# Performance work log

Measured on AMD Instinct MI355X. Metric: run time of the kernel, lower is better.

The kernel has to match this reference:

```python
import jax, jax.numpy as jnp
import numpy as np
import math

B = 4096
INPUT_SIZE = 2048
HIDDEN_SIZE = 2048


def setup_inputs() -> dict:
    key = jax.random.key(0)
    ks = jax.random.split(key, 7)
    std = 1.0 / math.sqrt(HIDDEN_SIZE)
    u = lambda k, shape: jax.random.uniform(k, shape, jnp.float32, -std, std)
    return {
        "input": jax.random.normal(ks[0], (B, INPUT_SIZE), jnp.float32),
        "hx": jax.random.normal(ks[1], (B, HIDDEN_SIZE), jnp.float32),
        "cx": jax.random.normal(ks[2], (B, HIDDEN_SIZE), jnp.float32),
        "W_x2h": u(ks[3], (4 * HIDDEN_SIZE, INPUT_SIZE)),
        "b_x2h": u(ks[4], (4 * HIDDEN_SIZE,)),
        "W_h2h": u(ks[5], (4 * HIDDEN_SIZE, HIDDEN_SIZE)),
        "b_h2h": u(ks[6], (4 * HIDDEN_SIZE,)),
    }


def reference(input, hx, cx, W_x2h, b_x2h, W_h2h, b_h2h):
    # gates: [B, 4H] = x @ W_x2h^T + b + h @ W_h2h^T + b
    gates = input @ W_x2h.T + b_x2h + hx @ W_h2h.T + b_h2h
    H = HIDDEN_SIZE
    ft = jax.nn.sigmoid(gates[:, 0 * H:1 * H])
    it = jax.nn.sigmoid(gates[:, 1 * H:2 * H])
    ct = jnp.tanh(gates[:, 2 * H:3 * H])
    ot = jax.nn.sigmoid(gates[:, 3 * H:4 * H])
    cy = ft * cx + it * ct
    hy = ot * jnp.tanh(cy)
    return (hy, cy)
```

## Files before the change

kernel.cpp:

```cpp
#include <hip/hip_runtime.h>
#include <hip/hip_bf16.h>


#define BATCH 4096
#define HID   2048
#define KDIM  2048
#define K4    4096
#define BM    128
#define BK    64
#define LDK   72

typedef __attribute__((ext_vector_type(8))) short  short8;
typedef __attribute__((ext_vector_type(4))) float  f32x4;

__device__ __forceinline__ float sigm(float x)  { return 1.f / (1.f + __expf(-x)); }
__device__ __forceinline__ float tanhx(float x) { return 2.f / (1.f + __expf(-2.f * x)) - 1.f; }

__device__ __forceinline__ uint2 pk_bf16x4(float4 v) {
  __hip_bfloat162 lo = __float22bfloat162_rn(make_float2(v.x, v.y));
  __hip_bfloat162 hi = __float22bfloat162_rn(make_float2(v.z, v.w));
  uint2 r;
  r.x = *(unsigned*)&lo;
  r.y = *(unsigned*)&hi;
  return r;
}

__device__ __forceinline__ void gload16(const void* g, void* l) {
  __builtin_amdgcn_global_load_lds(
      (const __attribute__((address_space(1))) unsigned int*)g,
      (__attribute__((address_space(3))) unsigned int*)l, 16, 0, 0);
}

__global__ __launch_bounds__(256) void conv_a(const float* __restrict__ X,
                                              const float* __restrict__ Hx,
                                              short* __restrict__ A) {
  const int gid = blockIdx.x * 256 + threadIdx.x;
  const int m   = gid >> 9;
  const int pos = (gid & 511) << 3;
  const float* src = (pos < KDIM) ? X  + (size_t)m * KDIM + pos
                                  : Hx + (size_t)m * KDIM + (pos - KDIM);
  float4 v0 = *(const float4*)src;
  float4 v1 = *(const float4*)(src + 4);
  uint2 p0 = pk_bf16x4(v0), p1 = pk_bf16x4(v1);
  uint4 o; o.x = p0.x; o.y = p0.y; o.z = p1.x; o.w = p1.y;
  *(uint4*)(A + (size_t)gid * 8) = o;
}

__global__ __launch_bounds__(256) void conv_b(const float* __restrict__ Wx,
                                              const float* __restrict__ Wh,
                                              short* __restrict__ Bm) {
  const int gid = blockIdx.x * 256 + threadIdx.x;
  const int jp  = gid >> 9;
  const int pos = (gid & 511) << 3;
  const int srow = (jp & 3) * HID + (jp >> 2);
  const float* src = (pos < KDIM) ? Wx + (size_t)srow * KDIM + pos
                                  : Wh + (size_t)srow * KDIM + (pos - KDIM);
  float4 v0 = *(const float4*)src;
  float4 v1 = *(const float4*)(src + 4);
  uint2 p0 = pk_bf16x4(v0), p1 = pk_bf16x4(v1);
  uint4 o; o.x = p0.x; o.y = p0.y; o.z = p1.x; o.w = p1.y;
  *(uint4*)(Bm + (size_t)gid * 8) = o;
}

__global__ __launch_bounds__(256) void lstm_mm(
    const short* __restrict__ A, const short* __restrict__ Bm,
    const float* __restrict__ Cx,
    const float* __restrict__ bx, const float* __restrict__ bh,
    float* __restrict__ Hy, float* __restrict__ Cy)
{
  __shared__ __align__(16) short A_lds[BM * BK];
  __shared__ __align__(16) short B_lds[BM * BK];

  const int tid  = threadIdx.x;
  const int wv   = tid >> 6;
  const int lane = tid & 63;
  const int quad = lane >> 4;
  const int ln   = lane & 15;
  const int wm   = wv >> 1;
  const int wn   = wv & 1;
  const int m0   = blockIdx.x * BM;
  const int j0   = blockIdx.y * BM;
  const int h0   = blockIdx.y * 32;

  f32x4 acc[4][4];
  #pragma unroll
  for (int a = 0; a < 4; ++a)
    #pragma unroll
    for (int b = 0; b < 4; ++b)
      acc[a][b] = (f32x4){0.f, 0.f, 0.f, 0.f};

  const int srow = lane >> 3;
  const int slot = lane & 7;
  const int sx   = ((slot ^ srow) << 3);
  const short* ag = A  + (size_t)(m0 + wv * 32 + srow) * K4 + sx;
  const short* bg = Bm + (size_t)(j0 + wv * 32 + srow) * K4 + sx;
  short* al = &A_lds[wv * 32 * BK];
  short* bl = &B_lds[wv * 32 * BK];

  for (int t = 0; t < K4 / BK; ++t) {
    const int k0 = t * BK;
    __syncthreads();
    #pragma unroll
    for (int i = 0; i < 4; ++i) {
      gload16(ag + k0 + i * 8 * K4, al + i * 8 * BK);
      gload16(bg + k0 + i * 8 * K4, bl + i * 8 * BK);
    }
    __syncthreads();
    #pragma unroll
    for (int ks = 0; ks < 2; ++ks) {
      short8 af[4], bfv[4];
      #pragma unroll
      for (int u = 0; u < 4; ++u) {
        const int ar = wm * 64 + u * 16 + ln;
        af[u]  = *(const short8*)&A_lds[ar * BK + (((ks * 4 + quad) ^ (ar & 7)) << 3)];
      }
      #pragma unroll
      for (int u = 0; u < 4; ++u) {
        const int br = wn * 64 + u * 16 + ln;
        bfv[u] = *(const short8*)&B_lds[br * BK + (((ks * 4 + quad) ^ (br & 7)) << 3)];
      }
      #pragma unroll
      for (int tm = 0; tm < 4; ++tm)
        #pragma unroll
        for (int tn = 0; tn < 4; ++tn)
          acc[tm][tn] = __builtin_amdgcn_mfma_f32_16x16x32_bf16(
              af[tm], bfv[tn], acc[tm][tn], 0, 0, 0);
    }
  }

  const int g = lane & 3;
  float biasv[4];
  int   hgs[4];
  #pragma unroll
  for (int tn = 0; tn < 4; ++tn) {
    int c  = wn * 64 + tn * 16 + ln;
    int hg = h0 + (c >> 2);
    hgs[tn] = hg;
    int j = g * HID + hg;
    biasv[tn] = bx[j] + bh[j];
  }
  #pragma unroll
  for (int tm = 0; tm < 4; ++tm) {
    #pragma unroll
    for (int r = 0; r < 4; ++r) {
      int mrow = m0 + wm * 64 + tm * 16 + quad * 4 + r;
      #pragma unroll
      for (int tn = 0; tn < 4; ++tn) {
        float v   = acc[tm][tn][r] + biasv[tn];
        float act = (g == 2) ? tanhx(v) : sigm(v);
        float y1 = __shfl_xor(act, 1);
        float y2 = __shfl_xor(act, 2);
        float y3 = __shfl_xor(act, 3);
        float ft = (g == 0) ? act : ((g == 1) ? y1 : ((g == 2) ? y2 : y3));
        float it = (g == 1) ? act : ((g == 0) ? y1 : ((g == 3) ? y2 : y3));
        float gt = (g == 2) ? act : ((g == 3) ? y1 : ((g == 0) ? y2 : y3));
        float ot = (g == 3) ? act : ((g == 2) ? y1 : ((g == 1) ? y2 : y3));
        if (g < 2) {
          size_t off = (size_t)mrow * HID + hgs[tn];
          float cxv = Cx[off];
          float cyv = ft * cxv + it * gt;
          if (g == 0) Hy[off] = ot * tanhx(cyv);
          else        Cy[off] = cyv;
        }
      }
    }
  }
}

__global__ __launch_bounds__(256) void lstm_cell_fallback(
    const float* __restrict__ X, const float* __restrict__ Hx,
    const float* __restrict__ Cx,
    const float* __restrict__ Wx, const float* __restrict__ bx,
    const float* __restrict__ Wh, const float* __restrict__ bh,
    float* __restrict__ Hy, float* __restrict__ Cy)
{
  __shared__ __align__(16) short A_lds[BM * LDK];
  __shared__ __align__(16) short B_lds[BM * LDK];

  const int tid  = threadIdx.x;
  const int wv   = tid >> 6;
  const int lane = tid & 63;
  const int quad = lane >> 4;
  const int ln   = lane & 15;
  const int wm   = wv >> 1;
  const int wn   = wv & 1;
  const int m0   = blockIdx.x * BM;
  const int h0   = blockIdx.y * 32;

  f32x4 acc[4][4];
  #pragma unroll
  for (int a = 0; a < 4; ++a)
    #pragma unroll
    for (int b = 0; b < 4; ++b)
      acc[a][b] = (f32x4){0.f, 0.f, 0.f, 0.f};

  const int rA  = tid >> 4;
  const int kc4 = (tid & 15) * 4;
  size_t aoff[8], boff[8];
  int    lrow[8];
  #pragma unroll
  for (int q = 0; q < 8; ++q) {
    int row  = q * 16 + rA;
    lrow[q]  = row;
    aoff[q]  = (size_t)(m0 + row) * KDIM + kc4;
    int wrow = (row & 3) * HID + h0 + (row >> 2);
    boff[q]  = (size_t)wrow * KDIM + kc4;
  }

  const int NT = 2 * (KDIM / BK);
  float4 areg[8], breg[8];
  #pragma unroll
  for (int q = 0; q < 8; ++q) {
    areg[q] = *(const float4*)(X  + aoff[q]);
    breg[q] = *(const float4*)(Wx + boff[q]);
  }

  for (int t = 0; t < NT; ++t) {
    __syncthreads();
    #pragma unroll
    for (int q = 0; q < 8; ++q) {
      *(uint2*)&A_lds[lrow[q] * LDK + kc4] = pk_bf16x4(areg[q]);
      *(uint2*)&B_lds[lrow[q] * LDK + kc4] = pk_bf16x4(breg[q]);
    }
    __syncthreads();
    if (t + 1 < NT) {
      const float* Ap = (t + 1 < 32) ? X  : Hx;
      const float* Wp = (t + 1 < 32) ? Wx : Wh;
      const int k0 = ((t + 1) & 31) * BK;
      #pragma unroll
      for (int q = 0; q < 8; ++q) {
        areg[q] = *(const float4*)(Ap + aoff[q] + k0);
        breg[q] = *(const float4*)(Wp + boff[q] + k0);
      }
    }
    #pragma unroll
    for (int ks = 0; ks < 2; ++ks) {
      short8 af[4], bfv[4];
      #pragma unroll
      for (int u = 0; u < 4; ++u)
        af[u] = *(const short8*)&A_lds[(wm * 64 + u * 16 + ln) * LDK + ks * 32 + quad * 8];
      #pragma unroll
      for (int u = 0; u < 4; ++u)
        bfv[u] = *(const short8*)&B_lds[(wn * 64 + u * 16 + ln) * LDK + ks * 32 + quad * 8];
      #pragma unroll
      for (int tm = 0; tm < 4; ++tm)
        #pragma unroll
        for (int tn = 0; tn < 4; ++tn)
          acc[tm][tn] = __builtin_amdgcn_mfma_f32_16x16x32_bf16(
              af[tm], bfv[tn], acc[tm][tn], 0, 0, 0);
    }
  }

  const int g = lane & 3;
  float biasv[4];
  int   hgs[4];
  #pragma unroll
  for (int tn = 0; tn < 4; ++tn) {
    int c  = wn * 64 + tn * 16 + ln;
    int hg = h0 + (c >> 2);
    hgs[tn] = hg;
    int j = g * HID + hg;
    biasv[tn] = bx[j] + bh[j];
  }
  #pragma unroll
  for (int tm = 0; tm < 4; ++tm) {
    #pragma unroll
    for (int r = 0; r < 4; ++r) {
      int mrow = m0 + wm * 64 + tm * 16 + quad * 4 + r;
      #pragma unroll
      for (int tn = 0; tn < 4; ++tn) {
        float v   = acc[tm][tn][r] + biasv[tn];
        float act = (g == 2) ? tanhx(v) : sigm(v);
        float y1 = __shfl_xor(act, 1);
        float y2 = __shfl_xor(act, 2);
        float y3 = __shfl_xor(act, 3);
        float ft = (g == 0) ? act : ((g == 1) ? y1 : ((g == 2) ? y2 : y3));
        float it = (g == 1) ? act : ((g == 0) ? y1 : ((g == 3) ? y2 : y3));
        float gt = (g == 2) ? act : ((g == 3) ? y1 : ((g == 0) ? y2 : y3));
        float ot = (g == 3) ? act : ((g == 2) ? y1 : ((g == 1) ? y2 : y3));
        if (g < 2) {
          size_t off = (size_t)mrow * HID + hgs[tn];
          float cxv = Cx[off];
          float cyv = ft * cxv + it * gt;
          if (g == 0) Hy[off] = ot * tanhx(cyv);
          else        Cy[off] = cyv;
        }
      }
    }
  }
}

extern "C" void kernel_launch(void* const* d_in, const int* in_sizes, int n_in,
                              void* d_out, int out_size, void* d_ws, size_t ws_size,
                              hipStream_t stream) {
  const float* X  = (const float*)d_in[0];
  const float* Hx = (const float*)d_in[1];
  const float* Cx = (const float*)d_in[2];
  const float* Wx = (const float*)d_in[3];
  const float* bx = (const float*)d_in[4];
  const float* Wh = (const float*)d_in[5];
  const float* bh = (const float*)d_in[6];
  float*       Hy = (float*)d_out;
  float*       Cy = Hy + (size_t)BATCH * HID;

  const size_t needA = (size_t)BATCH * K4 * sizeof(short);
  const size_t needB = (size_t)(4 * HID) * K4 * sizeof(short);

  if (d_ws != nullptr && ws_size >= needA + needB) {
    short* Abf = (short*)d_ws;
    short* Bbf = (short*)((char*)d_ws + needA);
    conv_a<<<dim3((BATCH * (K4 / 8)) / 256), dim3(256), 0, stream>>>(X, Hx, Abf);
    conv_b<<<dim3((4 * HID * (K4 / 8)) / 256), dim3(256), 0, stream>>>(Wx, Wh, Bbf);
    dim3 grid(BATCH / BM, HID / 32, 1);
    lstm_mm<<<grid, dim3(256, 1, 1), 0, stream>>>(Abf, Bbf, Cx, bx, bh, Hy, Cy);
  } else {
    dim3 grid(BATCH / BM, HID / 32, 1);
    lstm_cell_fallback<<<grid, dim3(256, 1, 1), 0, stream>>>(X, Hx, Cx, Wx, bx, Wh, bh, Hy, Cy);
  }
}
```

Measured before the change: 586.0 us.

## Replace GEMM with 256x256-tile 8-wave kernel using double-buffered LDS pipeline

Result: faster. 571.7 us (-2.4%).

```diff
diff --git a/kernel.cpp b/kernel.cpp
--- a/kernel.cpp
+++ b/kernel.cpp
@@ -6,8 +6,6 @@
 #define HID   2048
 #define KDIM  2048
 #define K4    4096
-#define BM    128
-#define BK    64
 #define LDK   72
 
 typedef __attribute__((ext_vector_type(8))) short  short8;
@@ -30,6 +28,10 @@
       (const __attribute__((address_space(1))) unsigned int*)g,
       (__attribute__((address_space(3))) unsigned int*)l, 16, 0, 0);
 }
+
+#define BAR()  asm volatile("s_barrier" ::: "memory")
+#define LGK0() asm volatile("s_waitcnt lgkmcnt(0)" ::: "memory")
+#define VMC(n) asm volatile("s_waitcnt vmcnt(" #n ")" ::: "memory")
 
 __global__ __launch_bounds__(256) void conv_a(const float* __restrict__ X,
                                               const float* __restrict__ Hx,
@@ -62,14 +64,190 @@
   *(uint4*)(Bm + (size_t)gid * 8) = o;
 }
 
-__global__ __launch_bounds__(256) void lstm_mm(
+__device__ __forceinline__ void lda4(short8 (&dst)[8], const short* base,
+                                     int arow, int sx0, int sx1, int mfb) {
+  #pragma unroll
+  for (int u = 0; u < 4; ++u) {
+    dst[u]     = *(const short8*)&base[arow + (mfb + u) * 1024 + sx0];
+    dst[4 + u] = *(const short8*)&base[arow + (mfb + u) * 1024 + sx1];
+  }
+}
+__device__ __forceinline__ void ldb2(short8 (&dst)[4], const short* base,
+                                     int brow, int sx0, int sx1, int nfb) {
+  #pragma unroll
+  for (int v = 0; v < 2; ++v) {
+    dst[v]     = *(const short8*)&base[brow + (nfb + v) * 1024 + sx0];
+    dst[2 + v] = *(const short8*)&base[brow + (nfb + v) * 1024 + sx1];
+  }
+}
+__device__ __forceinline__ void mmq(f32x4 (&acc)[8][4], const short8 (&A)[8],
+                                    const short8 (&B)[4], int MB, int NB) {
+  __builtin_amdgcn_s_setprio(1);
+  #pragma unroll
+  for (int ks = 0; ks < 2; ++ks)
+    #pragma unroll
+    for (int u = 0; u < 4; ++u)
+      #pragma unroll
+      for (int v = 0; v < 2; ++v)
+        acc[MB + u][NB + v] = __builtin_amdgcn_mfma_f32_16x16x32_bf16(
+            A[ks * 4 + u], B[ks * 2 + v], acc[MB + u][NB + v], 0, 0, 0);
+  __builtin_amdgcn_s_setprio(0);
+}
+
+__global__ __launch_bounds__(512, 2) void lstm_mm8(
     const short* __restrict__ A, const short* __restrict__ Bm,
     const float* __restrict__ Cx,
     const float* __restrict__ bx, const float* __restrict__ bh,
     float* __restrict__ Hy, float* __restrict__ Cy)
 {
-  __shared__ __align__(16) short A_lds[BM * BK];
-  __shared__ __align__(16) short B_lds[BM * BK];
+  __shared__ __align__(16) short A_sh[2 * 16384];
+  __shared__ __align__(16) short B_sh[2 * 16384];
+
+  const int tid  = threadIdx.x;
+  const int wv   = tid >> 6;
+  const int lane = tid & 63;
+  const int quad = lane >> 4;
+  const int ln   = lane & 15;
+  const int wm   = wv >> 2;
+  const int wn   = wv & 3;
+  const int m0   = blockIdx.x * 256;
+  const int j0   = blockIdx.y * 256;
+  const int h0   = blockIdx.y * 64;
+
+  f32x4 acc[8][4];
+  #pragma unroll
+  for (int a = 0; a < 8; ++a)
+    #pragma unroll
+    for (int b = 0; b < 4; ++b)
+      acc[a][b] = (f32x4){0.f, 0.f, 0.f, 0.f};
+
+  const int l8  = lane >> 3;
+  const int swz = ((lane & 7) ^ (l8 & 7)) << 3;
+  const short* aG = A  + (size_t)(m0 + l8) * K4 + swz;
+  const short* bG = Bm + (size_t)(j0 + l8) * K4 + swz;
+
+  #define STAGE_A(d, h, tau) do {                                             \
+    gload16(aG + ((size_t)((h)*128 + wv*16    )) * K4 + (tau)*64,             \
+            &A_sh[(d)*16384 + (h)*8192 + wv*1024]);                           \
+    gload16(aG + ((size_t)((h)*128 + wv*16 + 8)) * K4 + (tau)*64,             \
+            &A_sh[(d)*16384 + (h)*8192 + wv*1024 + 512]);                     \
+  } while (0)
+  #define STAGE_B(d, h, tau) do {                                             \
+    gload16(bG + ((size_t)((h)*128 + wv*16    )) * K4 + (tau)*64,             \
+            &B_sh[(d)*16384 + (h)*8192 + wv*1024]);                           \
+    gload16(bG + ((size_t)((h)*128 + wv*16 + 8)) * K4 + (tau)*64,             \
+            &B_sh[(d)*16384 + (h)*8192 + wv*1024 + 512]);                     \
+  } while (0)
+
+  const int arow = (wm * 128 + ln) * 64;
+  const int brow = (wn * 64  + ln) * 64;
+  const int sx0  = ((0 + quad) ^ (ln & 7)) << 3;
+  const int sx1  = ((4 + quad) ^ (ln & 7)) << 3;
+
+  STAGE_A(0, 0, 0); STAGE_A(0, 1, 0); STAGE_B(0, 0, 0); STAGE_B(0, 1, 0);
+  STAGE_A(1, 0, 1); STAGE_A(1, 1, 1); STAGE_B(1, 0, 1);
+  VMC(6);
+  BAR();
+
+  short8 aQ0[8], aQ1[8], bLo[4], bHi[4];
+
+  #pragma unroll 1
+  for (int i = 0; i < 32; ++i) {
+    const int  S0 = 2 * i + 2, S1 = 2 * i + 3, T1k = 2 * i + 1;
+    const bool nl = (i != 31);
+    lda4(aQ0, &A_sh[0], arow, sx0, sx1, 0);
+    ldb2(bLo, &B_sh[0], brow, sx0, sx1, 0);
+    STAGE_B(1, 1, T1k);
+    BAR(); LGK0();
+    mmq(acc, aQ0, bLo, 0, 0);
+    BAR();
+    lda4(aQ1, &A_sh[0], arow, sx0, sx1, 4);
+    BAR(); LGK0();
+    mmq(acc, aQ1, bLo, 4, 0);
+    BAR();
+    ldb2(bHi, &B_sh[0], brow, sx0, sx1, 2);
+    if (nl) STAGE_A(0, 0, S0);
+    BAR(); LGK0();
+    mmq(acc, aQ1, bHi, 4, 2);
+    BAR();
+    if (nl) STAGE_B(0, 0, S0);
+    BAR();
+    mmq(acc, aQ0, bHi, 0, 2);
+    if (nl) { VMC(4); } else { VMC(0); }
+    BAR();
+    lda4(aQ0, &A_sh[16384], arow, sx0, sx1, 0);
+    ldb2(bLo, &B_sh[16384], brow, sx0, sx1, 0);
+    if (nl) STAGE_A(0, 1, S0);
+    BAR(); LGK0();
+    mmq(acc, aQ0, bLo, 0, 0);
+    BAR();
+    lda4(aQ1, &A_sh[16384], arow, sx0, sx1, 4);
+    if (nl) STAGE_B(0, 1, S0);
+    BAR(); LGK0();
+    mmq(acc, aQ1, bLo, 4, 0);
+    BAR();
+    ldb2(bHi, &B_sh[16384], brow, sx0, sx1, 2);
+    if (nl) STAGE_A(1, 0, S1);
+    BAR(); LGK0();
+    mmq(acc, aQ1, bHi, 4, 2);
+    BAR();
+    if (nl) { STAGE_B(1, 0, S1); STAGE_A(1, 1, S1); }
+    BAR();
+    mmq(acc, aQ0, bHi, 0, 2);
+    if (nl) { VMC(6); }
+    BAR();
+  }
+  #undef STAGE_A
+  #undef STAGE_B
+
+  const int g = lane & 3;
+  float biasv[4];
+  int   hgs[4];
+  #pragma unroll
+  for (int nf = 0; nf < 4; ++nf) {
+    int c  = wn * 64 + nf * 16 + ln;
+    int hg = h0 + (c >> 2);
+    hgs[nf] = hg;
+    int j = g * HID + hg;
+    biasv[nf] = bx[j] + bh[j];
+  }
+  #pragma unroll
+  for (int mf = 0; mf < 8; ++mf) {
+    #pragma unroll
+    for (int r = 0; r < 4; ++r) {
+      int mrow = m0 + wm * 128 + mf * 16 + quad * 4 + r;
+      #pragma unroll
+      for (int nf = 0; nf < 4; ++nf) {
+        float v   = acc[mf][nf][r] + biasv[nf];
+        float act = (g == 2) ? tanhx(v) : sigm(v);
+        float y1 = __shfl_xor(act, 1);
+        float y2 = __shfl_xor(act, 2);
+        float y3 = __shfl_xor(act, 3);
+        float ft = (g == 0) ? act : ((g == 1) ? y1 : ((g == 2) ? y2 : y3));
+        float it = (g == 1) ? act : ((g == 0) ? y1 : ((g == 3) ? y2 : y3));
+        float gt = (g == 2) ? act : ((g == 3) ? y1 : ((g == 0) ? y2 : y3));
+        float ot = (g == 3) ? act : ((g == 2) ? y1 : ((g == 1) ? y2 : y3));
+        if (g < 2) {
+          size_t off = (size_t)mrow * HID + hgs[nf];
+          float cxv = Cx[off];
+          float cyv = ft * cxv + it * gt;
+          if (g == 0) Hy[off] = ot * tanhx(cyv);
+          else        Cy[off] = cyv;
+        }
+      }
+    }
+  }
+}
+
+__global__ __launch_bounds__(256) void lstm_cell_fallback(
+    const float* __restrict__ X, const float* __restrict__ Hx,
+    const float* __restrict__ Cx,
+    const float* __restrict__ Wx, const float* __restrict__ bx,
+    const float* __restrict__ Wh, const float* __restrict__ bh,
+    float* __restrict__ Hy, float* __restrict__ Cy)
+{
+  __shared__ __align__(16) short A_lds[128 * LDK];
+  __shared__ __align__(16) short B_lds[128 * LDK];
 
   const int tid  = threadIdx.x;
   const int wv   = tid >> 6;
@@ -78,8 +256,7 @@
   const int ln   = lane & 15;
   const int wm   = wv >> 1;
   const int wn   = wv & 1;
-  const int m0   = blockIdx.x * BM;
-  const int j0   = blockIdx.y * BM;
+  const int m0   = blockIdx.x * 128;
   const int h0   = blockIdx.y * 32;
 
   f32x4 acc[4][4];
@@ -89,36 +266,54 @@
     for (int b = 0; b < 4; ++b)
       acc[a][b] = (f32x4){0.f, 0.f, 0.f, 0.f};
 
-  const int srow = lane >> 3;
-  const int slot = lane & 7;
-  const int sx   = ((slot ^ srow) << 3);
-  const short* ag = A  + (size_t)(m0 + wv * 32 + srow) * K4 + sx;
-  const short* bg = Bm + (size_t)(j0 + wv * 32 + srow) * K4 + sx;
-  short* al = &A_lds[wv * 32 * BK];
-  short* bl = &B_lds[wv * 32 * BK];
-
-  for (int t = 0; t < K4 / BK; ++t) {
-    const int k0 = t * BK;
+  const int rA  = tid >> 4;
+  const int kc4 = (tid & 15) * 4;
+  size_t aoff[8], boff[8];
+  int    lrow[8];
+  #pragma unroll
+  for (int q = 0; q < 8; ++q) {
+    int row  = q * 16 + rA;
+    lrow[q]  = row;
+    aoff[q]  = (size_t)(m0 + row) * KDIM + kc4;
+    int wrow = (row & 3) * HID + h0 + (row >> 2);
+    boff[q]  = (size_t)wrow * KDIM + kc4;
+  }
+
+  const int NT = 2 * (KDIM / 64);
+  float4 areg[8], breg[8];
+  #pragma unroll
+  for (int q = 0; q < 8; ++q) {
+    areg[q] = *(const float4*)(X  + aoff[q]);
+    breg[q] = *(const float4*)(Wx + boff[q]);
+  }
+
+  for (int t = 0; t < NT; ++t) {
     __syncthreads();
     #pragma unroll
-    for (int i = 0; i < 4; ++i) {
-      gload16(ag + k0 + i * 8 * K4, al + i * 8 * BK);
-      gload16(bg + k0 + i * 8 * K4, bl + i * 8 * BK);
+    for (int q = 0; q < 8; ++q) {
+      *(uint2*)&A_lds[lrow[q] * LDK + kc4] = pk_bf16x4(areg[q]);
+      *(uint2*)&B_lds[lrow[q] * LDK + kc4] = pk_bf16x4(breg[q]);
     }
     __syncthreads();
+    if (t + 1 < NT) {
+      const float* Ap = (t + 1 < 32) ? X  : Hx;
+      const float* Wp = (t + 1 < 32) ? Wx : Wh;
+      const int k0 = ((t + 1) & 31) * 64;
+      #pragma unroll
+      for (int q = 0; q < 8; ++q) {
+        areg[q] = *(const float4*)(Ap + aoff[q] + k0);
+        breg[q] = *(const float4*)(Wp + boff[q] + k0);
+      }
+    }
     #pragma unroll
     for (int ks = 0; ks < 2; ++ks) {
       short8 af[4], bfv[4];
       #pragma unroll
-      for (int u = 0; u < 4; ++u) {
-        const int ar = wm * 64 + u * 16 + ln;
-        af[u]  = *(const short8*)&A_lds[ar * BK + (((ks * 4 + quad) ^ (ar & 7)) << 3)];
-      }
-      #pragma unroll
-      for (int u = 0; u < 4; ++u) {
-        const int br = wn * 64 + u * 16 + ln;
-        bfv[u] = *(const short8*)&B_lds[br * BK + (((ks * 4 + quad) ^ (br & 7)) << 3)];
-      }
+      for (int u = 0; u < 4; ++u)
+        af[u] = *(const short8*)&A_lds[(wm * 64 + u * 16 + ln) * LDK + ks * 32 + quad * 8];
+      #pragma unroll
+      for (int u = 0; u < 4; ++u)
+        bfv[u] = *(const short8*)&B_lds[(wn * 64 + u * 16 + ln) * LDK + ks * 32 + quad * 8];
       #pragma unroll
       for (int tm = 0; tm < 4; ++tm)
         #pragma unroll
@@ -167,129 +362,6 @@
   }
 }
 
-__global__ __launch_bounds__(256) void lstm_cell_fallback(
-    const float* __restrict__ X, const float* __restrict__ Hx,
-    const float* __restrict__ Cx,
-    const float* __restrict__ Wx, const float* __restrict__ bx,
-    const float* __restrict__ Wh, const float* __restrict__ bh,
-    float* __restrict__ Hy, float* __restrict__ Cy)
-{
-  __shared__ __align__(16) short A_lds[BM * LDK];
-  __shared__ __align__(16) short B_lds[BM * LDK];
-
-  const int tid  = threadIdx.x;
-  const int wv   = tid >> 6;
-  const int lane = tid & 63;
-  const int quad = lane >> 4;
-  const int ln   = lane & 15;
-  const int wm   = wv >> 1;
-  const int wn   = wv & 1;
-  const int m0   = blockIdx.x * BM;
-  const int h0   = blockIdx.y * 32;
-
-  f32x4 acc[4][4];
-  #pragma unroll
-  for (int a = 0; a < 4; ++a)
-    #pragma unroll
-    for (int b = 0; b < 4; ++b)
-      acc[a][b] = (f32x4){0.f, 0.f, 0.f, 0.f};
-
-  const int rA  = tid >> 4;
-  const int kc4 = (tid & 15) * 4;
-  size_t aoff[8], boff[8];
-  int    lrow[8];
-  #pragma unroll
-  for (int q = 0; q < 8; ++q) {
-    int row  = q * 16 + rA;
-    lrow[q]  = row;
-    aoff[q]  = (size_t)(m0 + row) * KDIM + kc4;
-    int wrow = (row & 3) * HID + h0 + (row >> 2);
-    boff[q]  = (size_t)wrow * KDIM + kc4;
-  }
-
-  const int NT = 2 * (KDIM / BK);
-  float4 areg[8], breg[8];
-  #pragma unroll
-  for (int q = 0; q < 8; ++q) {
-    areg[q] = *(const float4*)(X  + aoff[q]);
-    breg[q] = *(const float4*)(Wx + boff[q]);
-  }
-
-  for (int t = 0; t < NT; ++t) {
-    __syncthreads();
-    #pragma unroll
-    for (int q = 0; q < 8; ++q) {
-      *(uint2*)&A_lds[lrow[q] * LDK + kc4] = pk_bf16x4(areg[q]);
-      *(uint2*)&B_lds[lrow[q] * LDK + kc4] = pk_bf16x4(breg[q]);
-    }
-    __syncthreads();
-    if (t + 1 < NT) {
-      const float* Ap = (t + 1 < 32) ? X  : Hx;
-      const float* Wp = (t + 1 < 32) ? Wx : Wh;
-      const int k0 = ((t + 1) & 31) * BK;
-      #pragma unroll
-      for (int q = 0; q < 8; ++q) {
-        areg[q] = *(const float4*)(Ap + aoff[q] + k0);
-        breg[q] = *(const float4*)(Wp + boff[q] + k0);
-      }
-    }
-    #pragma unroll
-    for (int ks = 0; ks < 2; ++ks) {
-      short8 af[4], bfv[4];
-      #pragma unroll
-      for (int u = 0; u < 4; ++u)
-        af[u] = *(const short8*)&A_lds[(wm * 64 + u * 16 + ln) * LDK + ks * 32 + quad * 8];
-      #pragma unroll
-      for (int u = 0; u < 4; ++u)
-        bfv[u] = *(const short8*)&B_lds[(wn * 64 + u * 16 + ln) * LDK + ks * 32 + quad * 8];
-      #pragma unroll
-      for (int tm = 0; tm < 4; ++tm)
-        #pragma unroll
-        for (int tn = 0; tn < 4; ++tn)
-          acc[tm][tn] = __builtin_amdgcn_mfma_f32_16x16x32_bf16(
-              af[tm], bfv[tn], acc[tm][tn], 0, 0, 0);
-    }
-  }
-
-  const int g = lane & 3;
-  float biasv[4];
-  int   hgs[4];
-  #pragma unroll
-  for (int tn = 0; tn < 4; ++tn) {
-    int c  = wn * 64 + tn * 16 + ln;
-    int hg = h0 + (c >> 2);
-    hgs[tn] = hg;
-    int j = g * HID + hg;
-    biasv[tn] = bx[j] + bh[j];
-  }
-  #pragma unroll
-  for (int tm = 0; tm < 4; ++tm) {
-    #pragma unroll
-    for (int r = 0; r < 4; ++r) {
-      int mrow = m0 + wm * 64 + tm * 16 + quad * 4 + r;
-      #pragma unroll
-      for (int tn = 0; tn < 4; ++tn) {
-        float v   = acc[tm][tn][r] + biasv[tn];
-        float act = (g == 2) ? tanhx(v) : sigm(v);
-        float y1 = __shfl_xor(act, 1);
-        float y2 = __shfl_xor(act, 2);
-        float y3 = __shfl_xor(act, 3);
-        float ft = (g == 0) ? act : ((g == 1) ? y1 : ((g == 2) ? y2 : y3));
-        float it = (g == 1) ? act : ((g == 0) ? y1 : ((g == 3) ? y2 : y3));
-        float gt = (g == 2) ? act : ((g == 3) ? y1 : ((g == 0) ? y2 : y3));
-        float ot = (g == 3) ? act : ((g == 2) ? y1 : ((g == 1) ? y2 : y3));
-        if (g < 2) {
-          size_t off = (size_t)mrow * HID + hgs[tn];
-          float cxv = Cx[off];
-          float cyv = ft * cxv + it * gt;
-          if (g == 0) Hy[off] = ot * tanhx(cyv);
-          else        Cy[off] = cyv;
-        }
-      }
-    }
-  }
-}
-
 extern "C" void kernel_launch(void* const* d_in, const int* in_sizes, int n_in,
                               void* d_out, int out_size, void* d_ws, size_t ws_size,
                               hipStream_t stream) {
@@ -311,10 +383,10 @@
     short* Bbf = (short*)((char*)d_ws + needA);
     conv_a<<<dim3((BATCH * (K4 / 8)) / 256), dim3(256), 0, stream>>>(X, Hx, Abf);
     conv_b<<<dim3((4 * HID * (K4 / 8)) / 256), dim3(256), 0, stream>>>(Wx, Wh, Bbf);
-    dim3 grid(BATCH / BM, HID / 32, 1);
-    lstm_mm<<<grid, dim3(256, 1, 1), 0, stream>>>(Abf, Bbf, Cx, bx, bh, Hy, Cy);
+    dim3 grid(BATCH / 256, (4 * HID) / 256, 1);
+    lstm_mm8<<<grid, dim3(512, 1, 1), 0, stream>>>(Abf, Bbf, Cx, bx, bh, Hy, Cy);
   } else {
-    dim3 grid(BATCH / BM, HID / 32, 1);
+    dim3 grid(BATCH / 128, HID / 32, 1);
     lstm_cell_fallback<<<grid, dim3(256, 1, 1), 0, stream>>>(X, Hx, Cx, Wx, bx, Wh, bh, Hy, Cy);
   }
 }
```
